# Performance work log

Measured on AMD Instinct MI355X. Metric: run time of the kernel, lower is better.

## Reference

```python
import jax, jax.numpy as jnp
import numpy as np
from jax.ops import segment_sum

N_NODE, N_EDGE, D_IN, D_HID, N_CLS = 50000, 800000, 64, 64, 40


def setup_inputs() -> dict:
    key = jax.random.key(0)
    k1, k2, k3, k4 = jax.random.split(key, 4)
    x = jax.random.normal(k1, (N_NODE, D_IN), dtype=jnp.float32)
    edge_index = jax.random.randint(k2, (2, N_EDGE), 0, N_NODE, dtype=jnp.int64)
    W1 = jax.random.normal(k3, (D_IN, D_HID), dtype=jnp.float32) * (1.0 / np.sqrt(D_IN))
    b1 = jnp.zeros((D_HID,), dtype=jnp.float32)
    W2 = jax.random.normal(k4, (D_HID, N_CLS), dtype=jnp.float32) * (1.0 / np.sqrt(D_HID))
    b2 = jnp.zeros((N_CLS,), dtype=jnp.float32)
    return {"x": x, "edge_index": edge_index, "W1": W1, "b1": b1, "W2": W2, "b2": b2}


def _att_weights(fea, row, col, n):
    # edge-parallel cosine similarity (sklearn cosine_similarity restricted to edges)
    nrm = jnp.sqrt(jnp.sum(fea * fea, axis=1, keepdims=True))
    fn = fea / jnp.maximum(nrm, 1e-12)
    sim = jnp.sum(fn[row] * fn[col], axis=1)                 # [E]
    sim = jnp.where(sim < 0.1, 0.0, sim)                      # threshold
    # L1 row-normalization (sim >= 0 after threshold)
    rs = segment_sum(sim, row, num_segments=n)                # [N]
    sim_n = jnp.where(sim > 0, sim / jnp.maximum(rs[row], 1e-12), 0.0)
    # degree-based self-loop weight lam = 1/(deg+1)
    deg = segment_sum((sim > 0).astype(fea.dtype), row, num_segments=n)
    lam = 1.0 / (deg + 1.0)
    # exp applied only to stored (nonzero) entries; zeroed edges stay 0
    w_edge = jnp.where(sim > 0, jnp.exp(sim_n), 0.0)          # [E]
    w_self = jnp.exp(lam)                                     # [N] self-loop weights
    return w_edge, w_self


def _gcn(h, W, b, row, col, w_edge, w_self, n):
    # symmetric-norm GCN over weighted edges + explicit self loops
    deg = segment_sum(w_edge, row, num_segments=n) + w_self
    dinv = 1.0 / jnp.sqrt(jnp.maximum(deg, 1e-12))
    h = h @ W                                                 # [N, F]
    coef = w_edge * dinv[row] * dinv[col]                     # [E]
    out = segment_sum(coef[:, None] * h[col], row, num_segments=n)
    out = out + (w_self * dinv * dinv)[:, None] * h + b
    return out


def reference(x, edge_index, W1, b1, W2, b2):
    n = x.shape[0]
    row, col = edge_index[0], edge_index[1]
    # layer 1: attention coefs from raw features
    w1e, w1s = _att_weights(x, row, col, n)
    h = jax.nn.relu(_gcn(x, W1, b1, row, col, w1e, w1s, n))
    # layer 2: attention coefs recomputed on hidden features (dropout = eval mode)
    w2e, w2s = _att_weights(h, row, col, n)
    out = _gcn(h, W2, b2, row, col, w2e, w2s, n)
    return jax.nn.log_softmax(out, axis=1)
```

## Files before the change

### kernel.cpp

```cpp
#include <hip/hip_runtime.h>
#include <math.h>


#define ATT_CAP 96
#define EPB     2048
#define RPB     128
#define NBUCK_MAX 512
#define CAPB    4096

typedef _Float16 half4 __attribute__((ext_vector_type(4)));

__global__ void k_bscat_norm(const int* __restrict__ row, const int* __restrict__ col,
                             int* __restrict__ gcur, int* __restrict__ ebuf,
                             int E, int nbuck, int nblkA,
                             const float* __restrict__ x, float* __restrict__ fn, int N)
{
    __shared__ int lh[NBUCK_MAX];
    __shared__ int lbase[NBUCK_MAX];
    if ((int)blockIdx.x >= nblkA) {
        int gid  = (blockIdx.x - nblkA) * blockDim.x + threadIdx.x;
        int wid  = gid >> 6;
        int lane = threadIdx.x & 63;
        if (wid >= N) return;
        float v = x[(size_t)wid * 64 + lane];
        float s = v * v;
#pragma unroll
        for (int off = 32; off > 0; off >>= 1) s += __shfl_xor(s, off);
        float inv = 1.0f / fmaxf(sqrtf(s), 1e-12f);
        fn[(size_t)wid * 64 + lane] = v * inv;
        return;
    }
    int b = blockIdx.x;
    int ebeg = b * EPB;
    int rr[8], cc[8];
    for (int i = threadIdx.x; i < nbuck; i += blockDim.x) lh[i] = 0;
    __syncthreads();
#pragma unroll
    for (int k = 0; k < 8; ++k) {
        int e = ebeg + k * 256 + threadIdx.x;
        bool v = (e < E);
        int r = v ? row[e] : -1;
        int c = v ? col[e] : 0;
        rr[k] = r; cc[k] = c;
        if (v) atomicAdd(&lh[r >> 7], 1);
    }
    __syncthreads();
    for (int i = threadIdx.x; i < nbuck; i += blockDim.x) {
        int cnt = lh[i];
        if (cnt) lbase[i] = i * CAPB + atomicAdd(gcur + i, cnt);
        lh[i] = 0;
    }
    __syncthreads();
#pragma unroll
    for (int k = 0; k < 8; ++k) {
        int r = rr[k];
        if (r >= 0) {
            int j = r >> 7;
            int pos = lbase[j] + atomicAdd(&lh[j], 1);
            ebuf[pos] = ((r & (RPB - 1)) << 16) | cc[k];
        }
    }
}

__global__ void k_csr(const int* __restrict__ ebuf, const int* __restrict__ gcur,
                      int* __restrict__ rptr, int* __restrict__ col_s,
                      int N, int E, int nbuck)
{
    __shared__ int pk[CAPB];
    __shared__ int lcol[CAPB];
    __shared__ int lcnt[RPB], lexc[RPB], lcur[RPB];
    __shared__ int spart[4];
    int j = blockIdx.x;
    int tid = threadIdx.x;
    int lane = tid & 63, wave = tid >> 6;

    int part = 0;
    for (int i = tid; i < j; i += blockDim.x) part += gcur[i];
#pragma unroll
    for (int off = 32; off > 0; off >>= 1) part += __shfl_xor(part, off);
    if (lane == 0) spart[wave] = part;
    if (tid < RPB) lcnt[tid] = 0;
    __syncthreads();
    int beg = spart[0] + spart[1] + spart[2] + spart[3];
    int m = gcur[j]; if (m > CAPB) m = CAPB;

    const int* seg = ebuf + (size_t)j * CAPB;
    for (int i = tid; i < m; i += blockDim.x) pk[i] = seg[i];
    __syncthreads();
    for (int i = tid; i < m; i += blockDim.x) atomicAdd(&lcnt[pk[i] >> 16], 1);
    __syncthreads();
    if (tid < 64) {
        int a = lcnt[2 * tid], b2 = lcnt[2 * tid + 1];
        int s = a + b2;
        int incl = s;
#pragma unroll
        for (int off = 1; off < 64; off <<= 1) {
            int v = __shfl_up(incl, off);
            if (tid >= off) incl += v;
        }
        int base = incl - s;
        lexc[2 * tid] = base;     lexc[2 * tid + 1] = base + a;
        lcur[2 * tid] = base;     lcur[2 * tid + 1] = base + a;
    }
    __syncthreads();
    for (int i = tid; i < m; i += blockDim.x) {
        int v = pk[i];
        int p = atomicAdd(&lcur[v >> 16], 1);
        lcol[p] = v & 0xFFFF;
    }
    __syncthreads();
    for (int i = tid; i < m; i += blockDim.x) col_s[beg + i] = lcol[i];
    if (tid < RPB) {
        int r = j * RPB + tid;
        if (r < N) rptr[r] = beg + lexc[tid];
    }
    if (j == 0 && tid == 0) rptr[N] = E;
}

__global__ void k_att(const float* __restrict__ fn,
                      const int* __restrict__ rptr, const int* __restrict__ col_s,
                      int2* __restrict__ cw, int* __restrict__ lend,
                      float* __restrict__ dinv, float* __restrict__ selfc,
                      const float* __restrict__ g2, _Float16* __restrict__ hd2, int n)
{
    __shared__ float ssim[4][ATT_CAP];
    __shared__ int   scol[4][ATT_CAP];
    int wib  = threadIdx.x >> 6;
    int wid  = blockIdx.x * 4 + wib;
    int lane = threadIdx.x & 63;
    if (wid >= n) return;
    int sub = lane & 3;
    int grp = lane >> 2;
    int beg = rptr[wid], end = rptr[wid + 1];
    int deg_all = end - beg;

    const float4* frp = (const float4*)fn;
    unsigned rbase = (unsigned)wid * 16u;
    float4 a0 = frp[rbase + sub],     a1 = frp[rbase + sub + 4],
           a2 = frp[rbase + sub + 8], a3 = frp[rbase + sub + 12];

    float rs_part = 0.0f;
    int ngrp = (deg_all + 15) >> 4;
    for (int g = 0; g < ngrp; ++g) {
        int li = g * 16 + grp;
        float s = 0.0f; int c = 0;
        bool valid = (li < deg_all);
        if (valid) {
            c = col_s[beg + li];
            unsigned cb = (unsigned)c * 16u;
            float4 b0 = frp[cb + sub],     b1 = frp[cb + sub + 4],
                   b2 = frp[cb + sub + 8], b3 = frp[cb + sub + 12];
            float p = a0.x * b0.x + a0.y * b0.y + a0.z * b0.z + a0.w * b0.w
                    + a1.x * b1.x + a1.y * b1.y + a1.z * b1.z + a1.w * b1.w
                    + a2.x * b2.x + a2.y * b2.y + a2.z * b2.z + a2.w * b2.w
                    + a3.x * b3.x + a3.y * b3.y + a3.z * b3.z + a3.w * b3.w;
            p += __shfl_xor(p, 1);
            p += __shfl_xor(p, 2);
            s = (p < 0.1f) ? 0.0f : p;
        }
        if (sub == 0 && valid) {
            if (li < ATT_CAP) { ssim[wib][li] = s; scol[wib][li] = c; }
            if (s > 0.0f) rs_part += s;
        }
    }
#pragma unroll
    for (int off = 32; off > 0; off >>= 1) rs_part += __shfl_xor(rs_part, off);
    float denom = fmaxf(rs_part, 1e-12f);

    int   nlive = 0;
    float sw_lane = 0.0f;
    for (int base = 0; base < deg_all; base += 64) {
        int li = base + lane;
        bool valid = (li < deg_all);
        float s = 0.0f; int c = 0;
        if (valid) {
            if (li < ATT_CAP) { s = ssim[wib][li]; c = scol[wib][li]; }
            else {
                c = col_s[beg + li];
                const float* fr = fn + (size_t)wid * 64;
                const float* fc = fn + (size_t)c * 64;
                float p = 0.0f;
                for (int k = 0; k < 64; ++k) p += fr[k] * fc[k];
                s = (p < 0.1f) ? 0.0f : p;
            }
        }
        float w = (valid && s > 0.0f) ? expf(s / denom) : 0.0f;
        unsigned long long M = __ballot(w > 0.0f);
        int rank = __popcll(M & ((1ull << lane) - 1ull));
        if (w > 0.0f) {
            int2 pw; pw.x = c; pw.y = __float_as_int(w);
            cw[beg + nlive + rank] = pw;
            sw_lane += w;
        }
        nlive += __popcll(M);
    }
#pragma unroll
    for (int off = 32; off > 0; off >>= 1) sw_lane += __shfl_xor(sw_lane, off);

    float wself = expf(1.0f / ((float)nlive + 1.0f));
    float D  = sw_lane + wself;
    float di = rsqrtf(fmaxf(D, 1e-12f));
    if (lane == 0) {
        lend[wid]  = beg + nlive;
        dinv[wid]  = di;
        selfc[wid] = wself * di;
    }
    if (g2 && lane < 40)
        hd2[(size_t)wid * 40 + lane] = (_Float16)(g2[(size_t)wid * 40 + lane] * di);
}

template <int F, typename InT, typename OutT>
__global__ void k_gemm(const InT* __restrict__ fea, const float* __restrict__ W,
                       const float* __restrict__ scale, OutT* __restrict__ out, int n)
{
    constexpr int R = 256 / F;
    __shared__ float sW[64 * F];
    __shared__ float sX[R * 64];
    int tid = threadIdx.x;
    for (int i = tid; i < 64 * F; i += 256) sW[i] = W[i];
    int base = blockIdx.x * R;
    for (int i = tid; i < R * 64; i += 256) {
        int rr = base + i / 64;
        sX[i] = (rr < n) ? (float)fea[(size_t)rr * 64 + (i & 63)] : 0.0f;
    }
    __syncthreads();
    int rl = tid / F, j = tid % F;
    if (rl >= R) return;
    int r = base + rl;
    if (r >= n) return;
    float acc = 0.0f;
#pragma unroll
    for (int k = 0; k < 64; ++k) acc = fmaf(sX[rl * 64 + k], sW[k * F + j], acc);
    out[(size_t)r * F + j] = (OutT)(acc * scale[r]);
}

template <int F, typename Vec4>
__device__ inline float agg_core_t(const Vec4* __restrict__ hdv,
                                   const int2* __restrict__ cw,
                                   int beg, int lend_, int lane)
{
    int q  = lane & 15;
    int eg = lane >> 4;
    bool qact = (F == 64) ? true : (q < (F >> 2));
    constexpr unsigned FQ = F >> 2;
    float acc0 = 0.f, acc1 = 0.f, acc2 = 0.f, acc3 = 0.f;
    for (int base = beg; base < lend_; base += 64) {
        int idx = base + lane;
        int cv = 0; float wv = 0.0f;
        if (idx < lend_) { int2 pw = cw[(unsigned)idx]; cv = pw.x; wv = __int_as_float(pw.y); }
        int cnt = lend_ - base; if (cnt > 64) cnt = 64;
        int nit = (cnt + 3) >> 2;

        Vec4  hv[4] = {};
        float wj[4] = {};
#pragma unroll
        for (int p = 0; p < 4; ++p) {
            int c = __shfl(cv, 4 * p + eg);
            wj[p] = __shfl(wv, 4 * p + eg);
            if (qact && p < nit) hv[p] = hdv[(unsigned)c * FQ + (unsigned)q];
        }
#pragma unroll
        for (int it = 0; it < 16; ++it) {
            if (it < nit) {
                float w = wj[it & 3];
                Vec4  h = hv[it & 3];
                acc0 += w * (float)h.x;
                acc1 += w * (float)h.y;
                acc2 += w * (float)h.z;
                acc3 += w * (float)h.w;
                if (it + 4 < nit) {
                    int jn = 4 * (it + 4);
                    int c = __shfl(cv, jn + eg);
                    wj[it & 3] = __shfl(wv, jn + eg);
                    if (qact) hv[it & 3] = hdv[(unsigned)c * FQ + (unsigned)q];
                }
            }
        }
    }
    acc0 += __shfl_xor(acc0, 16); acc0 += __shfl_xor(acc0, 32);
    acc1 += __shfl_xor(acc1, 16); acc1 += __shfl_xor(acc1, 32);
    acc2 += __shfl_xor(acc2, 16); acc2 += __shfl_xor(acc2, 32);
    acc3 += __shfl_xor(acc3, 16); acc3 += __shfl_xor(acc3, 32);
    int srcq = lane >> 2;
    float a0 = __shfl(acc0, srcq);
    float a1 = __shfl(acc1, srcq);
    float a2 = __shfl(acc2, srcq);
    float a3 = __shfl(acc3, srcq);
    int k = lane & 3;
    return (k == 0) ? a0 : (k == 1) ? a1 : (k == 2) ? a2 : a3;
}

__global__ void k_agg64(const float* __restrict__ hd, const int2* __restrict__ cw,
                        const float* __restrict__ dinv, const float* __restrict__ selfc,
                        const float* __restrict__ b, const int* __restrict__ row_ptr,
                        const int* __restrict__ lend, const float* __restrict__ W2,
                        float* __restrict__ g2, float* __restrict__ fnh, int n)
{
    __shared__ float sW2[64 * 40];
    __shared__ float sv[4][64];
    int tid = threadIdx.x;
    {
        const float4* W4 = (const float4*)W2;
        float4* s4 = (float4*)sW2;
        for (int i = tid; i < 64 * 40 / 4; i += 256) s4[i] = W4[i];
    }
    __syncthreads();

    int lane = tid & 63;
    int wib  = tid >> 6;
    float bl = b[lane];
    for (int t = 0; t < 2; ++t) {
        int wid = blockIdx.x * 8 + wib * 2 + t;
        if (wid >= n) break;
        int beg = row_ptr[wid], le = lend[wid];
        float hs = hd[(unsigned)wid * 64u + (unsigned)lane];
        float dv = dinv[wid];
        float sc = selfc[wid];
        float accf = agg_core_t<64>((const float4*)hd, cw, beg, le, lane);
        float v = dv * accf + sc * hs + bl;
        v = fmaxf(v, 0.0f);
        float s = v * v;
#pragma unroll
        for (int off = 32; off > 0; off >>= 1) s += __shfl_xor(s, off);
        float inv = 1.0f / fmaxf(sqrtf(s), 1e-12f);
        fnh[(unsigned)wid * 64u + (unsigned)lane] = v * inv;

        sv[wib][lane] = v;
        if (lane < 40) {
            float acc = 0.0f;
#pragma unroll
            for (int k = 0; k < 64; ++k) acc = fmaf(sv[wib][k], sW2[k * 40 + lane], acc);
            g2[(unsigned)wid * 40u + (unsigned)lane] = acc;
        }
    }
}

__global__ void k_agg40_lsm(const _Float16* __restrict__ hd2, const int2* __restrict__ cw,
                            const float* __restrict__ dinv, const float* __restrict__ selfc,
                            const float* __restrict__ b, const int* __restrict__ row_ptr,
                            const int* __restrict__ lend,
                            float* __restrict__ out, int n)
{
    constexpr int F = 40;
    int gid  = blockIdx.x * blockDim.x + threadIdx.x;
    int wid  = gid >> 6;
    int lane = threadIdx.x & 63;
    if (wid >= n) return;
    int beg = row_ptr[wid], le = lend[wid];
    bool active = (lane < F);
    float hs = active ? (float)hd2[(unsigned)wid * 40u + (unsigned)lane] : 0.0f;
    float dv = dinv[wid];
    float sc = selfc[wid];
    float bl = active ? b[lane] : 0.0f;
    float accf = agg_core_t<F>((const half4*)hd2, cw, beg, le, lane);
    float v = 0.0f;
    if (active) v = dv * accf + sc * hs + bl;
    float m = active ? v : -__builtin_inff();
#pragma unroll
    for (int off = 32; off > 0; off >>= 1) m = fmaxf(m, __shfl_xor(m, off));
    float ex = active ? expf(v - m) : 0.0f;
    float s = ex;
#pragma unroll
    for (int off = 32; off > 0; off >>= 1) s += __shfl_xor(s, off);
    if (active) out[(size_t)wid * F + lane] = v - m - logf(s);
}

extern "C" void kernel_launch(void* const* d_in, const int* in_sizes, int n_in,
                              void* d_out, int out_size, void* d_ws, size_t ws_size,
                              hipStream_t stream)
{
    const float* x  = (const float*)d_in[0];
    const int*   ei = (const int*)d_in[1];
    const float* W1 = (const float*)d_in[2];
    const float* b1 = (const float*)d_in[3];
    const float* W2 = (const float*)d_in[4];
    const float* b2 = (const float*)d_in[5];
    float* out = (float*)d_out;

    const int N = in_sizes[0] / 64;
    const int E = in_sizes[1] / 2;
    const int* row = ei;
    const int* col = ei + E;

    const int nblkA = (E + EPB - 1) / EPB;
    const int nbuck = (N + RPB - 1) / RPB;

    char* p = (char*)d_ws;
    auto alloc = [&](size_t bytes) -> char* {
        char* r = p; p += (bytes + 255) & ~(size_t)255; return r;
    };
    float*     fn     = (float*)alloc((size_t)N * 64 * 4);
    float*     dinv   = (float*)alloc((size_t)N * 4);
    float*     selfc  = (float*)alloc((size_t)N * 4);
    float*     hd1    = (float*)alloc((size_t)N * 64 * 4);
    float*     g2     = (float*)alloc((size_t)N * 40 * 4);
    _Float16*  hd2    = (_Float16*)alloc((size_t)N * 40 * 2);
    float*     fnh    = (float*)alloc((size_t)N * 64 * 4);
    int*       rptr   = (int*)alloc((size_t)(N + 1) * 4);
    int*       lendv  = (int*)alloc((size_t)N * 4);
    int*       col_s  = (int*)alloc((size_t)E * 4);
    int2*      cw     = (int2*)alloc((size_t)E * 8);
    int*       ebuf   = (int*)alloc((size_t)nbuck * CAPB * 4);
    int*       gcur   = (int*)alloc((size_t)nbuck * 4);

    const int TB = 256;
    int blk_nodeWave = (N * 64 + TB - 1) / TB;
    int blk_node4    = (N + 3) / 4;
    int blk_node8    = (N + 7) / 8;

    hipMemsetAsync(gcur, 0, (size_t)nbuck * 4, stream);

    k_bscat_norm<<<nblkA + blk_nodeWave, TB, 0, stream>>>(row, col, gcur, ebuf,
                                                          E, nbuck, nblkA, x, fn, N);
    k_csr<<<nbuck, TB, 0, stream>>>(ebuf, gcur, rptr, col_s, N, E, nbuck);

    k_att<<<blk_node4, TB, 0, stream>>>(fn, rptr, col_s, cw, lendv, dinv, selfc,
                                        (const float*)nullptr, (_Float16*)nullptr, N);
    k_gemm<64, float, float><<<(N + 3) / 4, TB, 0, stream>>>(x, W1, dinv, hd1, N);
    k_agg64<<<blk_node8, TB, 0, stream>>>(hd1, cw, dinv, selfc, b1,
                                          rptr, lendv, W2, g2, fnh, N);

    k_att<<<blk_node4, TB, 0, stream>>>(fnh, rptr, col_s, cw, lendv, dinv, selfc,
                                        g2, hd2, N);
    k_agg40_lsm<<<blk_nodeWave, TB, 0, stream>>>(hd2, cw, dinv, selfc, b2,
                                                 rptr, lendv, out, N);
}
```

Measured before the change: 255.2 us.

## Fold layer-1 GEMM into bucket-scatter kernel and apply dinv scaling in attention

Moves the unscaled x@W1 product into the first combined kernel as extra blocks, so it runs alongside the edge bucketing and row normalisation. The later attention kernel then multiplies the hd1 rows by dinv in place, and the separate GEMM launch is removed. It also switches to fast-math intrinsics (__expf, __logf, rsqrtf) and 32-bit index arithmetic. The fused kernel now reserves 16KB of shared memory for W in every block, scatter blocks included, which can reduce occupancy. hd1 also makes an extra read-modify-write pass.

```diff
diff --git a/kernel.cpp b/kernel.cpp
--- a/kernel.cpp
+++ b/kernel.cpp
@@ -10,34 +10,61 @@
 
 typedef _Float16 half4 __attribute__((ext_vector_type(4)));
 
-__global__ void k_bscat_norm(const int* __restrict__ row, const int* __restrict__ col,
-                             int* __restrict__ gcur, int* __restrict__ ebuf,
-                             int E, int nbuck, int nblkA,
-                             const float* __restrict__ x, float* __restrict__ fn, int N)
+__global__ void k_bscat_norm_gemm(const int* __restrict__ row, const int* __restrict__ col,
+                                  int* __restrict__ gcur, int* __restrict__ ebuf,
+                                  int E, int nbuck, int nblkA, int nblkB,
+                                  const float* __restrict__ x, float* __restrict__ fn,
+                                  const float* __restrict__ W1, float* __restrict__ hd1,
+                                  int N)
 {
     __shared__ int lh[NBUCK_MAX];
     __shared__ int lbase[NBUCK_MAX];
-    if ((int)blockIdx.x >= nblkA) {
-        int gid  = (blockIdx.x - nblkA) * blockDim.x + threadIdx.x;
+    __shared__ float sW[64 * 64];
+    __shared__ float sX[4 * 64];
+    int b = blockIdx.x;
+    int tid = threadIdx.x;
+    if (b >= nblkA + nblkB) {
+        int gb = b - nblkA - nblkB;
+        const float4* W4 = (const float4*)W1;
+        float4* s4 = (float4*)sW;
+#pragma unroll
+        for (int i = 0; i < 4; ++i) s4[tid + 256 * i] = W4[tid + 256 * i];
+        int base = gb * 4;
+        {
+            int rr = base + (tid >> 6);
+            sX[tid] = (rr < N) ? x[(unsigned)rr * 64u + (unsigned)(tid & 63)] : 0.0f;
+        }
+        __syncthreads();
+        int rl = tid >> 6, j = tid & 63;
+        int r = base + rl;
+        if (r < N) {
+            float acc = 0.0f;
+#pragma unroll
+            for (int k = 0; k < 64; ++k) acc = fmaf(sX[rl * 64 + k], sW[k * 64 + j], acc);
+            hd1[(unsigned)r * 64u + (unsigned)j] = acc;
+        }
+        return;
+    }
+    if (b >= nblkA) {
+        int gid  = (b - nblkA) * blockDim.x + tid;
         int wid  = gid >> 6;
-        int lane = threadIdx.x & 63;
+        int lane = tid & 63;
         if (wid >= N) return;
-        float v = x[(size_t)wid * 64 + lane];
+        float v = x[(unsigned)wid * 64u + (unsigned)lane];
         float s = v * v;
 #pragma unroll
         for (int off = 32; off > 0; off >>= 1) s += __shfl_xor(s, off);
-        float inv = 1.0f / fmaxf(sqrtf(s), 1e-12f);
-        fn[(size_t)wid * 64 + lane] = v * inv;
+        float inv = rsqrtf(fmaxf(s, 1e-24f));
+        fn[(unsigned)wid * 64u + (unsigned)lane] = v * inv;
         return;
     }
-    int b = blockIdx.x;
     int ebeg = b * EPB;
     int rr[8], cc[8];
-    for (int i = threadIdx.x; i < nbuck; i += blockDim.x) lh[i] = 0;
+    for (int i = tid; i < nbuck; i += blockDim.x) lh[i] = 0;
     __syncthreads();
 #pragma unroll
     for (int k = 0; k < 8; ++k) {
-        int e = ebeg + k * 256 + threadIdx.x;
+        int e = ebeg + k * 256 + tid;
         bool v = (e < E);
         int r = v ? row[e] : -1;
         int c = v ? col[e] : 0;
@@ -45,7 +72,7 @@
         if (v) atomicAdd(&lh[r >> 7], 1);
     }
     __syncthreads();
-    for (int i = threadIdx.x; i < nbuck; i += blockDim.x) {
+    for (int i = tid; i < nbuck; i += blockDim.x) {
         int cnt = lh[i];
         if (cnt) lbase[i] = i * CAPB + atomicAdd(gcur + i, cnt);
         lh[i] = 0;
@@ -121,7 +148,8 @@
                       const int* __restrict__ rptr, const int* __restrict__ col_s,
                       int2* __restrict__ cw, int* __restrict__ lend,
                       float* __restrict__ dinv, float* __restrict__ selfc,
-                      const float* __restrict__ g2, _Float16* __restrict__ hd2, int n)
+                      const float* __restrict__ g2, _Float16* __restrict__ hd2,
+                      float* __restrict__ hsc, int n)
 {
     __shared__ float ssim[4][ATT_CAP];
     __shared__ int   scol[4][ATT_CAP];
@@ -184,7 +212,7 @@
                 s = (p < 0.1f) ? 0.0f : p;
             }
         }
-        float w = (valid && s > 0.0f) ? expf(s / denom) : 0.0f;
+        float w = (valid && s > 0.0f) ? __expf(s / denom) : 0.0f;
         unsigned long long M = __ballot(w > 0.0f);
         int rank = __popcll(M & ((1ull << lane) - 1ull));
         if (w > 0.0f) {
@@ -197,7 +225,7 @@
 #pragma unroll
     for (int off = 32; off > 0; off >>= 1) sw_lane += __shfl_xor(sw_lane, off);
 
-    float wself = expf(1.0f / ((float)nlive + 1.0f));
+    float wself = __expf(1.0f / ((float)nlive + 1.0f));
     float D  = sw_lane + wself;
     float di = rsqrtf(fmaxf(D, 1e-12f));
     if (lane == 0) {
@@ -205,33 +233,11 @@
         dinv[wid]  = di;
         selfc[wid] = wself * di;
     }
+    if (hsc)
+        hsc[(unsigned)wid * 64u + (unsigned)lane] *= di;
     if (g2 && lane < 40)
-        hd2[(size_t)wid * 40 + lane] = (_Float16)(g2[(size_t)wid * 40 + lane] * di);
-}
-
-template <int F, typename InT, typename OutT>
-__global__ void k_gemm(const InT* __restrict__ fea, const float* __restrict__ W,
-                       const float* __restrict__ scale, OutT* __restrict__ out, int n)
-{
-    constexpr int R = 256 / F;
-    __shared__ float sW[64 * F];
-    __shared__ float sX[R * 64];
-    int tid = threadIdx.x;
-    for (int i = tid; i < 64 * F; i += 256) sW[i] = W[i];
-    int base = blockIdx.x * R;
-    for (int i = tid; i < R * 64; i += 256) {
-        int rr = base + i / 64;
-        sX[i] = (rr < n) ? (float)fea[(size_t)rr * 64 + (i & 63)] : 0.0f;
-    }
-    __syncthreads();
-    int rl = tid / F, j = tid % F;
-    if (rl >= R) return;
-    int r = base + rl;
-    if (r >= n) return;
-    float acc = 0.0f;
-#pragma unroll
-    for (int k = 0; k < 64; ++k) acc = fmaf(sX[rl * 64 + k], sW[k * F + j], acc);
-    out[(size_t)r * F + j] = (OutT)(acc * scale[r]);
+        hd2[(unsigned)wid * 40u + (unsigned)lane] =
+            (_Float16)(g2[(unsigned)wid * 40u + (unsigned)lane] * di);
 }
 
 template <int F, typename Vec4>
@@ -322,7 +328,7 @@
         float s = v * v;
 #pragma unroll
         for (int off = 32; off > 0; off >>= 1) s += __shfl_xor(s, off);
-        float inv = 1.0f / fmaxf(sqrtf(s), 1e-12f);
+        float inv = rsqrtf(fmaxf(s, 1e-24f));
         fnh[(unsigned)wid * 64u + (unsigned)lane] = v * inv;
 
         sv[wib][lane] = v;
@@ -358,11 +364,11 @@
     float m = active ? v : -__builtin_inff();
 #pragma unroll
     for (int off = 32; off > 0; off >>= 1) m = fmaxf(m, __shfl_xor(m, off));
-    float ex = active ? expf(v - m) : 0.0f;
+    float ex = active ? __expf(v - m) : 0.0f;
     float s = ex;
 #pragma unroll
     for (int off = 32; off > 0; off >>= 1) s += __shfl_xor(s, off);
-    if (active) out[(size_t)wid * F + lane] = v - m - logf(s);
+    if (active) out[(size_t)wid * F + lane] = v - m - __logf(s);
 }
 
 extern "C" void kernel_launch(void* const* d_in, const int* in_sizes, int n_in,
@@ -405,23 +411,24 @@
 
     const int TB = 256;
     int blk_nodeWave = (N * 64 + TB - 1) / TB;
+    int blk_gemm     = (N + 3) / 4;
     int blk_node4    = (N + 3) / 4;
     int blk_node8    = (N + 7) / 8;
 
     hipMemsetAsync(gcur, 0, (size_t)nbuck * 4, stream);
 
-    k_bscat_norm<<<nblkA + blk_nodeWave, TB, 0, stream>>>(row, col, gcur, ebuf,
-                                                          E, nbuck, nblkA, x, fn, N);
+    k_bscat_norm_gemm<<<nblkA + blk_nodeWave + blk_gemm, TB, 0, stream>>>(
+        row, col, gcur, ebuf, E, nbuck, nblkA, blk_nodeWave, x, fn, W1, hd1, N);
     k_csr<<<nbuck, TB, 0, stream>>>(ebuf, gcur, rptr, col_s, N, E, nbuck);
 
     k_att<<<blk_node4, TB, 0, stream>>>(fn, rptr, col_s, cw, lendv, dinv, selfc,
-                                        (const float*)nullptr, (_Float16*)nullptr, N);
-    k_gemm<64, float, float><<<(N + 3) / 4, TB, 0, stream>>>(x, W1, dinv, hd1, N);
+                                        (const float*)nullptr, (_Float16*)nullptr,
+                                        hd1, N);
     k_agg64<<<blk_node8, TB, 0, stream>>>(hd1, cw, dinv, selfc, b1,
                                           rptr, lendv, W2, g2, fnh, N);
 
     k_att<<<blk_node4, TB, 0, stream>>>(fnh, rptr, col_s, cw, lendv, dinv, selfc,
-                                        g2, hd2, N);
+                                        g2, hd2, (float*)nullptr, N);
     k_agg40_lsm<<<blk_nodeWave, TB, 0, stream>>>(hd2, cw, dinv, selfc, b2,
                                                  rptr, lendv, out, N);
 }
```

Measured after the change: 251.9 us (median of 3 runs). No clear change (-1.3%).
